# Performance work log

Hardware: AMD Instinct MI355X
Metric: run time of the kernel (lower is better)

Reference implementation:

```python
import jax, jax.numpy as jnp
import numpy as np

KS, STRIDE, PAD, GROUPS = 7, 1, 3, 8


def setup_inputs() -> dict:
    key = jax.random.key(0)
    ks = jax.random.split(key, 6)
    B, C, H, W = 4, 128, 64, 64
    O = 128
    rel_size = O // GROUPS // 2  # 8
    return {
        "x": jax.random.normal(ks[0], (B, C, H, W), jnp.float32),
        "wq": jax.random.normal(ks[1], (O, C), jnp.float32) * 0.05,
        "wk": jax.random.normal(ks[2], (O, C), jnp.float32) * 0.05,
        "wv": jax.random.normal(ks[3], (O, C), jnp.float32) * 0.05,
        "rel_x": jax.random.normal(ks[4], (rel_size, KS), jnp.float32),
        "rel_y": jax.random.normal(ks[5], (O // GROUPS - rel_size, KS), jnp.float32),
    }


def _patches(a, fH, fW):
    # a: [B, C, pH, pW] -> [B, C, fH, fW, KS, KS] (overlapping windows, like torch unfold)
    cols = []
    for ki in range(KS):
        rows = []
        for kj in range(KS):
            rows.append(a[:, :, ki:ki + (fH - 1) * STRIDE + 1:STRIDE,
                             kj:kj + (fW - 1) * STRIDE + 1:STRIDE])
        cols.append(jnp.stack(rows, axis=-1))  # last axis = l (W-kernel)
    return jnp.stack(cols, axis=-2)            # second-to-last = k (H-kernel)


def reference(x, wq, wk, wv, rel_x, rel_y):
    B, C, H, W = x.shape
    O = wq.shape[0]
    rel_size = rel_x.shape[0]
    xp = jnp.pad(x, ((0, 0), (0, 0), (PAD, PAD), (PAD, PAD)))
    pH, pW = H + 2 * PAD, W + 2 * PAD
    fH, fW = (pH - KS) // STRIDE + 1, (pW - KS) // STRIDE + 1
    # 1x1 convs
    q = jnp.einsum('oc,bchw->bohw', wq, xp)
    k = jnp.einsum('oc,bchw->bohw', wk, xp)
    v = jnp.einsum('oc,bchw->bohw', wv, xp)
    h0 = (KS - 1) // 2
    win_q = q[:, :, h0:pH - KS // 2:STRIDE, h0:pW - KS // 2:STRIDE]  # [B,O,fH,fW]
    win_q_b = win_q.reshape(B, GROUPS, O // GROUPS, fH, fW)
    qx = win_q_b[:, :, :rel_size]
    qy = win_q_b[:, :, rel_size:]
    bias_x = jnp.einsum('bgxhw,xk->bhwk', qx, rel_x)  # varies along l (W-kernel)
    bias_y = jnp.einsum('bgyhw,yk->bhwk', qy, rel_y)  # varies along k (H-kernel)
    win_k = _patches(k, fH, fW)  # [B,O,fH,fW,KS,KS]
    win_v = _patches(v, fH, fW)
    logits = jnp.einsum('bchw,bchwkl->bhwkl', win_q, win_k)
    logits = logits + bias_x[:, :, :, None, :] + bias_y[:, :, :, :, None]
    attn = jax.nn.softmax(logits.reshape(B, fH, fW, KS * KS), axis=-1)
    attn = attn.reshape(B, fH, fW, KS, KS)
    out = jnp.einsum('bhwkl,bchwkl->bchw', attn, win_v)  # [B,O,fH,fW]
    return out
```

## Files before the change

kernel.cpp:

```cpp
#include <hip/hip_runtime.h>

typedef __fp16 half8_t __attribute__((ext_vector_type(8)));
typedef float  f4_t    __attribute__((ext_vector_type(4)));

__device__ __forceinline__ unsigned pk(float a, float b) {
    return __builtin_bit_cast(unsigned, __builtin_amdgcn_cvt_pkrtz(a, b));
}

__global__ __launch_bounds__(256) void qkv_direct(
    const float* __restrict__ x, const float* __restrict__ wq,
    const float* __restrict__ wk, const float* __restrict__ wv,
    const float* __restrict__ relx, const float* __restrict__ rely,
    unsigned* __restrict__ qf, unsigned* __restrict__ kf,
    unsigned* __restrict__ vf, float* __restrict__ biasG)
{
    __shared__ float sS[4][320];
    __shared__ float relsQ[120];

    const int tid = threadIdx.x, wvn = tid >> 6, lane = tid & 63;
    const int mtx = blockIdx.x >> 8;
    const int tg  = blockIdx.x & 255;
    const float* wsrc = (mtx == 0) ? wq : (mtx == 1 ? wk : wv);
    unsigned*    dst  = (mtx == 0) ? qf : (mtx == 1 ? kf : vf);

    if (mtx == 0 && tid < 120)
        relsQ[tid] = (tid < 56) ? relx[tid] : (tid < 112 ? rely[tid - 56] : 0.f);

    const int m = lane & 15, quad = lane >> 4;

    const int t = tg * 4 + wvn;
    const int p0 = t * 16, b = p0 >> 12, hw = p0 & 4095;
    const float* xb = x + (size_t)b * (128 * 4096) + hw + m;
    half8_t B[4];
#pragma unroll
    for (int ck = 0; ck < 4; ++ck) {
        float f[8];
#pragma unroll
        for (int j = 0; j < 8; ++j) f[j] = xb[(size_t)(ck * 32 + quad * 8 + j) * 4096];
        unsigned* d = (unsigned*)&B[ck];
        d[0] = pk(f[0], f[1]); d[1] = pk(f[2], f[3]);
        d[2] = pk(f[4], f[5]); d[3] = pk(f[6], f[7]);
    }

    float s0 = 0.f, s1 = 0.f, s2 = 0.f, s3 = 0.f;
    unsigned* dpx = dst + (size_t)(p0 + m) * 64 + quad * 2;
#pragma unroll
    for (int og = 0; og < 8; ++og) {
        half8_t A[4];
#pragma unroll
        for (int kc = 0; kc < 4; ++kc) {
            const float* wr = wsrc + (size_t)(og * 16 + m) * 128 + kc * 32 + quad * 8;
            const float4 w0 = *(const float4*)wr;
            const float4 w1 = *(const float4*)(wr + 4);
            unsigned* d = (unsigned*)&A[kc];
            d[0] = pk(w0.x, w0.y); d[1] = pk(w0.z, w0.w);
            d[2] = pk(w1.x, w1.y); d[3] = pk(w1.z, w1.w);
        }
        f4_t acc = {0.f, 0.f, 0.f, 0.f};
#pragma unroll
        for (int kc = 0; kc < 4; ++kc)
            acc = __builtin_amdgcn_mfma_f32_16x16x32_f16(A[kc], B[kc], acc, 0, 0, 0);
        if (mtx == 0) { s0 += acc[0]; s1 += acc[1]; s2 += acc[2]; s3 += acc[3]; }
        *(uint2*)(dpx + og * 8) = make_uint2(pk(acc[0], acc[1]), pk(acc[2], acc[3]));
    }

    if (mtx == 0) {
        __syncthreads();
        float* sw = sS[wvn];
        *(f4_t*)&sw[m * 20 + quad * 4] = (f4_t){s0, s1, s2, s3};
        __asm__ volatile("s_waitcnt lgkmcnt(0)" ::: "memory");
        __builtin_amdgcn_wave_barrier();
        f4_t bj = {0.f, 0.f, 0.f, 0.f};
#pragma unroll
        for (int jj = 0; jj < 4; ++jj) {
            const int j = quad * 4 + jj;
            float s = 0.f;
            if (j < 7) {
#pragma unroll
                for (int tt = 0; tt < 8; ++tt)
                    s = fmaf(sw[m * 20 + tt], relsQ[tt * 7 + j], s);
            } else if (j < 14) {
#pragma unroll
                for (int tt = 0; tt < 8; ++tt)
                    s = fmaf(sw[m * 20 + 8 + tt], relsQ[56 + tt * 7 + (j - 7)], s);
            }
            bj[jj] = s;
        }
        *(f4_t*)(biasG + (size_t)(p0 + m) * 16 + quad * 4) = bj;
    }
}

constexpr int VP = 168;

__global__ __launch_bounds__(256) void attn_mfma(
    const unsigned* __restrict__ qf, const unsigned* __restrict__ kf,
    const unsigned* __restrict__ vf, const float* __restrict__ biasG,
    float* __restrict__ out)
{
    __shared__ __fp16 vH[128 * VP];
    __shared__ __fp16 aW[2][16 * 136];
    __shared__ float  biasL[32 * 16];

    const int tid = threadIdx.x, bx = blockIdx.x;
    const int wv = tid >> 6, lane = tid & 63;
    const int w0 = (bx & 7) * 8;
    const int h0 = ((bx >> 3) & 15) * 4;
    const int b  = bx >> 7;
    const int s  = wv >> 1, u = wv & 1;
    const int wr = h0 + 2 * s + u;
    const int n16 = lane & 15, quad = lane >> 4;

    for (int i = tid; i < 2176; i += 256) ((unsigned*)aW)[i] = 0u;

    {
        const int g = tid >> 3, r = tid & 7;
#pragma unroll
        for (int it = 0; it < 5; ++it) {
            const int pq = r + 8 * it;
            const int hi = pq >> 2, ciq = pq & 3;
            const int py = h0 - 3 + hi;
            unsigned d0[4], d1[4];
#pragma unroll
            for (int p = 0; p < 4; ++p) {
                const int pxc = w0 - 3 + ciq * 4 + p;
                uint2 d = make_uint2(0u, 0u);
                if ((unsigned)py < 64u && (unsigned)pxc < 64u)
                    d = *(const uint2*)(vf + (size_t)((b * 4096 + py * 64 + pxc) * 64 + g * 2));
                d0[p] = d.x; d1[p] = d.y;
            }
            const int c0 = g * 4, off = hi * 16 + ciq * 4;
            *(uint2*)(vH + (c0 + 0) * VP + off) = make_uint2(
                __builtin_amdgcn_perm(d0[1], d0[0], 0x05040100u),
                __builtin_amdgcn_perm(d0[3], d0[2], 0x05040100u));
            *(uint2*)(vH + (c0 + 1) * VP + off) = make_uint2(
                __builtin_amdgcn_perm(d0[1], d0[0], 0x07060302u),
                __builtin_amdgcn_perm(d0[3], d0[2], 0x07060302u));
            *(uint2*)(vH + (c0 + 2) * VP + off) = make_uint2(
                __builtin_amdgcn_perm(d1[1], d1[0], 0x05040100u),
                __builtin_amdgcn_perm(d1[3], d1[2], 0x05040100u));
            *(uint2*)(vH + (c0 + 3) * VP + off) = make_uint2(
                __builtin_amdgcn_perm(d1[1], d1[0], 0x07060302u),
                __builtin_amdgcn_perm(d1[3], d1[2], 0x07060302u));
        }
    }

    for (int i = tid; i < 512; i += 256) {
        const int px = i >> 4, tt = i & 15;
        const int pix = b * 4096 + (h0 + (px >> 3)) * 64 + w0 + (px & 7);
        biasL[px * 16 + tt] = biasG[(size_t)pix * 16 + tt];
    }
    __syncthreads();

    uint4 qA[4];
    {
        const bool vm = n16 < 8;
        const size_t qb = (size_t)(b * 4096 + wr * 64 + w0 + n16) * 64;
#pragma unroll
        for (int kc = 0; kc < 4; ++kc) {
            uint4 t4 = make_uint4(0u, 0u, 0u, 0u);
            if (vm) t4 = *(const uint4*)(qf + qb + kc * 16 + quad * 4);
            qA[kc] = t4;
        }
    }
    f4_t lg[7];
#pragma unroll
    for (int t = 0; t < 7; ++t) {
        const int py = wr - 3 + t;
        const int pxc = w0 - 3 + n16;
        const bool val = ((unsigned)py < 64u) && ((unsigned)pxc < 64u);
        const size_t kb = (size_t)(b * 4096 + py * 64 + pxc) * 64;
        f4_t acc = {0.f, 0.f, 0.f, 0.f};
#pragma unroll
        for (int kc = 0; kc < 4; ++kc) {
            uint4 kB = make_uint4(0u, 0u, 0u, 0u);
            if (val) kB = *(const uint4*)(kf + kb + kc * 16 + quad * 4);
            acc = __builtin_amdgcn_mfma_f32_16x16x32_f16(
                __builtin_bit_cast(half8_t, qA[kc]),
                __builtin_bit_cast(half8_t, kB), acc, 0, 0, 0);
        }
        lg[t] = acc;
    }

    const int rowblk = 2 * s + u;
#pragma unroll
    for (int i = 0; i < 4; ++i) {
        const int m = quad * 4 + i;
        const float* bb = &biasL[(rowblk * 8 + (m & 7)) * 16];
        const int kj = n16 - m;
        const bool kv = (unsigned)kj < 7u;
        const float bx2 = kv ? bb[kj] : 0.f;
        float lv[7];
        float mx = -1e30f;
#pragma unroll
        for (int t = 0; t < 7; ++t) {
            const float v = kv ? lg[t][i] + bx2 + bb[7 + t] : -1e30f;
            lv[t] = v;
            mx = fmaxf(mx, v);
        }
        mx = fmaxf(mx, __shfl_xor(mx, 1));
        mx = fmaxf(mx, __shfl_xor(mx, 2));
        mx = fmaxf(mx, __shfl_xor(mx, 4));
        mx = fmaxf(mx, __shfl_xor(mx, 8));
        float ss = 0.f;
#pragma unroll
        for (int t = 0; t < 7; ++t) {
            const float e = __expf(lv[t] - mx);
            lv[t] = e;
            ss += e;
        }
        ss += __shfl_xor(ss, 1);
        ss += __shfl_xor(ss, 2);
        ss += __shfl_xor(ss, 4);
        ss += __shfl_xor(ss, 8);
        const float inv = 1.f / ss;
        if (m < 8) {
            __fp16* wp = &aW[s][(u * 8 + m) * 136];
#pragma unroll
            for (int t = 0; t < 7; ++t)
                wp[(u + t) * 16 + n16] = (__fp16)(lv[t] * inv);
        }
    }
    __syncthreads();

    uint4 pA[4];
#pragma unroll
    for (int kc = 0; kc < 4; ++kc)
        pA[kc] = *(const uint4*)(&aW[s][n16 * 136 + kc * 32 + quad * 8]);
#pragma unroll
    for (int tt = 0; tt < 4; ++tt) {
        const int tn = u * 4 + tt;
        f4_t acc = {0.f, 0.f, 0.f, 0.f};
#pragma unroll
        for (int kc = 0; kc < 4; ++kc) {
            const int kri = kc * 2 + (quad >> 1);
            const int ci0 = (quad & 1) * 8;
            const half8_t vB = *(const half8_t*)(
                vH + (tn * 16 + n16) * VP + (2 * s + kri) * 16 + ci0);
            acc = __builtin_amdgcn_mfma_f32_16x16x32_f16(
                __builtin_bit_cast(half8_t, pA[kc]), vB, acc, 0, 0, 0);
        }
        const int c = tn * 16 + n16;
        float* ob = out + (size_t)(b * 128 + c) * 4096;
#pragma unroll
        for (int i = 0; i < 4; ++i) {
            const int mm = quad * 4 + i;
            ob[(h0 + 2 * s + (mm >> 3)) * 64 + w0 + (mm & 7)] = acc[i];
        }
    }
}

extern "C" void kernel_launch(void* const* d_in, const int* in_sizes, int n_in,
                              void* d_out, int out_size, void* d_ws, size_t ws_size,
                              hipStream_t stream) {
    const float* x    = (const float*)d_in[0];
    const float* wq   = (const float*)d_in[1];
    const float* wk   = (const float*)d_in[2];
    const float* wv   = (const float*)d_in[3];
    const float* relx = (const float*)d_in[4];
    const float* rely = (const float*)d_in[5];
    float* out = (float*)d_out;

    char* ws = (char*)d_ws;
    unsigned* qfb = (unsigned*)(ws);
    unsigned* kfb = (unsigned*)(ws + 0x400000);
    unsigned* vfb = (unsigned*)(ws + 0x800000);
    float*    bG  = (float*)   (ws + 0xC00000);

    qkv_direct<<<dim3(768), 256, 0, stream>>>(x, wq, wk, wv, relx, rely,
                                              qfb, kfb, vfb, bG);
    attn_mfma<<<dim3(512), 256, 0, stream>>>(qfb, kfb, vfb, bG, out);
}
```

Before: 113.6 us.

## Stage weights and input tile in shared memory for QKV projection

The QKV kernel now converts the whole weight matrix to fp16 once per block into LDS, laid out in MFMA fragment order. It also loads a 128x64 input tile with coalesced float4 loads into padded LDS instead of strided scalar global reads per lane. This removes repeated per-wave global weight loads and conversions and the uncoalesced x reads. In exchange it uses about 66KB of LDS per block, which may lower occupancy, and adds a block-wide barrier before compute.

```diff
diff --git a/kernel.cpp b/kernel.cpp
--- a/kernel.cpp
+++ b/kernel.cpp
@@ -7,15 +7,17 @@
     return __builtin_bit_cast(unsigned, __builtin_amdgcn_cvt_pkrtz(a, b));
 }
 
-__global__ __launch_bounds__(256) void qkv_direct(
+__global__ __launch_bounds__(256) void qkv_tile(
     const float* __restrict__ x, const float* __restrict__ wq,
     const float* __restrict__ wk, const float* __restrict__ wv,
     const float* __restrict__ relx, const float* __restrict__ rely,
     unsigned* __restrict__ qf, unsigned* __restrict__ kf,
     unsigned* __restrict__ vf, float* __restrict__ biasG)
 {
-    __shared__ float sS[4][320];
-    __shared__ float relsQ[120];
+    __shared__ __fp16 Af[2048 * 8];
+    __shared__ float  xS[128 * 66];
+    __shared__ float  sS[4][320];
+    __shared__ float  relsQ[120];
 
     const int tid = threadIdx.x, wvn = tid >> 6, lane = tid & 63;
     const int mtx = blockIdx.x >> 8;
@@ -26,46 +28,59 @@
     if (mtx == 0 && tid < 120)
         relsQ[tid] = (tid < 56) ? relx[tid] : (tid < 112 ? rely[tid - 56] : 0.f);
 
+#pragma unroll
+    for (int s = 0; s < 8; ++s) {
+        const int it = s * 256 + tid;
+        const int l = it & 63, ck = (it >> 6) & 3, ot = it >> 8;
+        const float* wr = wsrc + (size_t)(ot * 16 + (l & 15)) * 128 + ck * 32 + (l >> 4) * 8;
+        const float4 w0 = *(const float4*)wr;
+        const float4 w1 = *(const float4*)(wr + 4);
+        unsigned* d = (unsigned*)&Af[it * 8];
+        d[0] = pk(w0.x, w0.y); d[1] = pk(w0.z, w0.w);
+        d[2] = pk(w1.x, w1.y); d[3] = pk(w1.z, w1.w);
+    }
+
+    const int b   = tg >> 6;
+    const int hw0 = (tg & 63) * 64;
+    const float* xbase = x + (size_t)b * (128 * 4096) + hw0;
+#pragma unroll
+    for (int it = 0; it < 8; ++it) {
+        const int i = it * 256 + tid;
+        const int c = i >> 4, f4i = i & 15;
+        const float4 v4 = *(const float4*)(xbase + (size_t)c * 4096 + f4i * 4);
+        *(float4*)&xS[c * 66 + f4i * 4] = v4;
+    }
+    __syncthreads();
+
     const int m = lane & 15, quad = lane >> 4;
-
-    const int t = tg * 4 + wvn;
-    const int p0 = t * 16, b = p0 >> 12, hw = p0 & 4095;
-    const float* xb = x + (size_t)b * (128 * 4096) + hw + m;
+    const int pxl = wvn * 16 + m;
     half8_t B[4];
 #pragma unroll
     for (int ck = 0; ck < 4; ++ck) {
         float f[8];
 #pragma unroll
-        for (int j = 0; j < 8; ++j) f[j] = xb[(size_t)(ck * 32 + quad * 8 + j) * 4096];
+        for (int j = 0; j < 8; ++j) f[j] = xS[(ck * 32 + quad * 8 + j) * 66 + pxl];
         unsigned* d = (unsigned*)&B[ck];
         d[0] = pk(f[0], f[1]); d[1] = pk(f[2], f[3]);
         d[2] = pk(f[4], f[5]); d[3] = pk(f[6], f[7]);
     }
 
+    const int p0g = tg * 64 + wvn * 16;
     float s0 = 0.f, s1 = 0.f, s2 = 0.f, s3 = 0.f;
-    unsigned* dpx = dst + (size_t)(p0 + m) * 64 + quad * 2;
+    unsigned* dpx = dst + (size_t)(p0g + m) * 64 + quad * 2;
 #pragma unroll
     for (int og = 0; og < 8; ++og) {
-        half8_t A[4];
-#pragma unroll
-        for (int kc = 0; kc < 4; ++kc) {
-            const float* wr = wsrc + (size_t)(og * 16 + m) * 128 + kc * 32 + quad * 8;
-            const float4 w0 = *(const float4*)wr;
-            const float4 w1 = *(const float4*)(wr + 4);
-            unsigned* d = (unsigned*)&A[kc];
-            d[0] = pk(w0.x, w0.y); d[1] = pk(w0.z, w0.w);
-            d[2] = pk(w1.x, w1.y); d[3] = pk(w1.z, w1.w);
-        }
         f4_t acc = {0.f, 0.f, 0.f, 0.f};
 #pragma unroll
-        for (int kc = 0; kc < 4; ++kc)
-            acc = __builtin_amdgcn_mfma_f32_16x16x32_f16(A[kc], B[kc], acc, 0, 0, 0);
+        for (int kc = 0; kc < 4; ++kc) {
+            const half8_t A = *(const half8_t*)&Af[((og * 4 + kc) * 64 + lane) * 8];
+            acc = __builtin_amdgcn_mfma_f32_16x16x32_f16(A, B[kc], acc, 0, 0, 0);
+        }
         if (mtx == 0) { s0 += acc[0]; s1 += acc[1]; s2 += acc[2]; s3 += acc[3]; }
         *(uint2*)(dpx + og * 8) = make_uint2(pk(acc[0], acc[1]), pk(acc[2], acc[3]));
     }
 
     if (mtx == 0) {
-        __syncthreads();
         float* sw = sS[wvn];
         *(f4_t*)&sw[m * 20 + quad * 4] = (f4_t){s0, s1, s2, s3};
         __asm__ volatile("s_waitcnt lgkmcnt(0)" ::: "memory");
@@ -86,7 +101,7 @@
             }
             bj[jj] = s;
         }
-        *(f4_t*)(biasG + (size_t)(p0 + m) * 16 + quad * 4) = bj;
+        *(f4_t*)(biasG + (size_t)(p0g + m) * 16 + quad * 4) = bj;
     }
 }
 
@@ -266,7 +281,7 @@
     unsigned* vfb = (unsigned*)(ws + 0x800000);
     float*    bG  = (float*)   (ws + 0xC00000);
 
-    qkv_direct<<<dim3(768), 256, 0, stream>>>(x, wq, wk, wv, relx, rely,
-                                              qfb, kfb, vfb, bG);
+    qkv_tile<<<dim3(768), 256, 0, stream>>>(x, wq, wk, wv, relx, rely,
+                                            qfb, kfb, vfb, bG);
     attn_mfma<<<dim3(512), 256, 0, stream>>>(qfb, kfb, vfb, bG, out);
 }
```

New measurement: 101.5 us. 10.7% less time.
